# Performance work log

Measured on AMD Instinct MI355X. Metric: run time of the kernel, lower is better.

The kernel has to match this reference:

```python
import jax, jax.numpy as jnp
import numpy as np

D = 1024          # label_size / in_features
V = 100000        # vocab size
SHORTLIST = 10000 # cutoffs[0]
# tail clusters: (proj_dim, cluster_size) per div_value=2 schedule
TAILS = [(512, 10000), (256, 20000), (128, 40000), (64, 20000)]


def setup_inputs() -> dict:
    key = jax.random.key(0)
    ks = jax.random.split(key, 11)
    s = jnp.float32(0.02)
    inp = {
        "feature": jax.random.normal(ks[0], (D,), jnp.float32),
        "targets": jax.random.randint(ks[1], (4096,), 0, V),
        "head_w": jax.random.normal(ks[2], (SHORTLIST + len(TAILS), D), jnp.float32) * s,
    }
    for i, (h, c) in enumerate(TAILS):
        inp[f"t{i}p"] = jax.random.normal(ks[3 + 2 * i], (h, D), jnp.float32) * s
        inp[f"t{i}w"] = jax.random.normal(ks[4 + 2 * i], (c, h), jnp.float32) * s
    return inp


def reference(feature, targets, head_w, t0p, t0w, t1p, t1w, t2p, t2w, t3p, t3w):
    # head logits: [SHORTLIST + n_clusters]
    head_lp = jax.nn.log_softmax(head_w @ feature)
    parts = [head_lp[:SHORTLIST]]
    tails = [(t0p, t0w), (t1p, t1w), (t2p, t2w), (t3p, t3w)]
    for i, (p, w) in enumerate(tails):
        # two-stage low-rank projection: [h] then cluster logits [c]
        cl_lp = jax.nn.log_softmax(w @ (p @ feature)) + head_lp[SHORTLIST + i]
        parts.append(cl_lp)
    logprob = jnp.concatenate(parts)  # [V] full-vocab log-probabilities
    return -jnp.mean(logprob[targets])
```

## Files before the change

kernel.cpp:

```cpp
#include <hip/hip_runtime.h>
#include <math.h>

#define NHEAD     10004
#define OFF_HEAD  0
#define OFF_H0    10004
#define OFF_H1    10516
#define OFF_H2    10772
#define OFF_H3    10900
#define OFF_C0    10964
#define OFF_C1    20964
#define OFF_C2    40964
#define OFF_C3    80964
#define OFF_PH    100964
#define OFF_P0    101590
#define OFF_P1    102215
#define OFF_P2    103465
#define OFF_P3    105965

__device__ __forceinline__ float wave_sum(float v) {
  v += __shfl_xor(v, 32, 64);
  v += __shfl_xor(v, 16, 64);
  v += __shfl_xor(v, 8, 64);
  v += __shfl_xor(v, 4, 64);
  v += __shfl_xor(v, 2, 64);
  v += __shfl_xor(v, 1, 64);
  return v;
}

__global__ __launch_bounds__(256) void head_proj_kernel(
    const float* __restrict__ feat, const float* __restrict__ head_w,
    const float* __restrict__ p0, const float* __restrict__ p1,
    const float* __restrict__ p2, const float* __restrict__ p3,
    float* __restrict__ ws) {
  __shared__ __align__(16) float sf[1024];
  ((float4*)sf)[threadIdx.x] = ((const float4*)feat)[threadIdx.x];
  __syncthreads();
  const float4* sf4 = (const float4*)sf;
  const int wave = threadIdx.x >> 6, lane = threadIdx.x & 63;
  const int b = blockIdx.x;

  if (b < 626) {
    float esum = 0.f;
#pragma unroll
    for (int k = 0; k < 4; ++k) {
      int row = b * 16 + wave * 4 + k;
      if (row < NHEAD) {
        const float4* src4 = (const float4*)head_w + (size_t)row * 256;
        float acc = 0.f;
#pragma unroll
        for (int j = 0; j < 4; ++j) {
          float4 a = src4[lane + j * 64];
          float4 c = sf4[lane + j * 64];
          acc += a.x * c.x + a.y * c.y + a.z * c.z + a.w * c.w;
        }
        acc = wave_sum(acc);
        if (lane == 0) { ws[OFF_HEAD + row] = acc; esum += expf(acc); }
      }
    }
    __shared__ float wred[4];
    if (lane == 0) wred[wave] = esum;
    __syncthreads();
    if (threadIdx.x == 0) ws[OFF_PH + b] = wred[0] + wred[1] + wred[2] + wred[3];
  } else {
    const int pb = b - 626;
#pragma unroll
    for (int k = 0; k < 4; ++k) {
      int row = NHEAD + pb * 16 + wave * 4 + k;
      const float* src;
      if (row < 10516)      src = p0 + (size_t)(row - 10004) * 1024;
      else if (row < 10772) src = p1 + (size_t)(row - 10516) * 1024;
      else if (row < 10900) src = p2 + (size_t)(row - 10772) * 1024;
      else                  src = p3 + (size_t)(row - 10900) * 1024;
      const float4* src4 = (const float4*)src;
      float acc = 0.f;
#pragma unroll
      for (int j = 0; j < 4; ++j) {
        float4 a = src4[lane + j * 64];
        float4 c = sf4[lane + j * 64];
        acc += a.x * c.x + a.y * c.y + a.z * c.z + a.w * c.w;
      }
      acc = wave_sum(acc);
      if (lane == 0) ws[row] = acc;
    }
  }
}

__global__ __launch_bounds__(256) void tail_kernel(
    const float* __restrict__ w0, const float* __restrict__ w1,
    const float* __restrict__ w2, const float* __restrict__ w3,
    float* __restrict__ ws) {
  __shared__ __align__(16) float sh[512];
  const int b = blockIdx.x;
  const float* w; int h, hoff, coff, poff, lb;
  if (b < 625)       { w = w0; h = 512; hoff = OFF_H0; coff = OFF_C0; poff = OFF_P0; lb = b; }
  else if (b < 1875) { w = w1; h = 256; hoff = OFF_H1; coff = OFF_C1; poff = OFF_P1; lb = b - 625; }
  else if (b < 4375) { w = w2; h = 128; hoff = OFF_H2; coff = OFF_C2; poff = OFF_P2; lb = b - 1875; }
  else               { w = w3; h = 64;  hoff = OFF_H3; coff = OFF_C3; poff = OFF_P3; lb = b - 4375; }
  for (int t = threadIdx.x; t < h; t += 256) sh[t] = ws[hoff + t];
  __syncthreads();
  const int wave = threadIdx.x >> 6, lane = threadIdx.x & 63;
  const int row0 = lb * 16 + wave * 4;
  float esum = 0.f;
#pragma unroll
  for (int k = 0; k < 4; ++k) {
    int row = row0 + k;
    const float* wr = w + (size_t)row * h;
    float acc = 0.f;
    if (h == 512) {
      const float4* wr4 = (const float4*)wr; const float4* sh4 = (const float4*)sh;
#pragma unroll
      for (int j = 0; j < 2; ++j) {
        float4 a = wr4[lane + j * 64]; float4 c = sh4[lane + j * 64];
        acc += a.x * c.x + a.y * c.y + a.z * c.z + a.w * c.w;
      }
    } else if (h == 256) {
      float4 a = ((const float4*)wr)[lane]; float4 c = ((const float4*)sh)[lane];
      acc = a.x * c.x + a.y * c.y + a.z * c.z + a.w * c.w;
    } else if (h == 128) {
      float2 a = ((const float2*)wr)[lane]; float2 c = ((const float2*)sh)[lane];
      acc = a.x * c.x + a.y * c.y;
    } else {
      acc = wr[lane] * sh[lane];
    }
    acc = wave_sum(acc);
    if (lane == 0) { ws[coff + row] = acc; esum += expf(acc); }
  }
  __shared__ float wred[4];
  if (lane == 0) wred[wave] = esum;
  __syncthreads();
  if (threadIdx.x == 0) ws[poff + lb] = wred[0] + wred[1] + wred[2] + wred[3];
}

__global__ __launch_bounds__(256) void finalize_kernel(
    const int* __restrict__ targets, const float* __restrict__ ws,
    float* __restrict__ out) {
  __shared__ float red[256];
  float lse[5];
  const int offs[5] = {OFF_PH, OFF_P0, OFF_P1, OFF_P2, OFF_P3};
  const int lens[5] = {626, 625, 1250, 2500, 1250};
  for (int s = 0; s < 5; ++s) {
    float v = 0.f;
    for (int i = threadIdx.x; i < lens[s]; i += 256) v += ws[offs[s] + i];
    red[threadIdx.x] = v; __syncthreads();
    for (int st = 128; st; st >>= 1) {
      if (threadIdx.x < st) red[threadIdx.x] += red[threadIdx.x + st];
      __syncthreads();
    }
    lse[s] = logf(red[0]);
    __syncthreads();
  }
  const float clh0 = ws[10000] - lse[0];
  const float clh1 = ws[10001] - lse[0];
  const float clh2 = ws[10002] - lse[0];
  const float clh3 = ws[10003] - lse[0];
  float s = 0.f;
  for (int i = threadIdx.x; i < 4096; i += 256) {
    int t = targets[i]; float lp;
    if (t < 10000)      lp = ws[OFF_HEAD + t] - lse[0];
    else if (t < 20000) lp = ws[OFF_C0 + t - 10000] - lse[1] + clh0;
    else if (t < 40000) lp = ws[OFF_C1 + t - 20000] - lse[2] + clh1;
    else if (t < 80000) lp = ws[OFF_C2 + t - 40000] - lse[3] + clh2;
    else                lp = ws[OFF_C3 + t - 80000] - lse[4] + clh3;
    s += lp;
  }
  red[threadIdx.x] = s; __syncthreads();
  for (int st = 128; st; st >>= 1) {
    if (threadIdx.x < st) red[threadIdx.x] += red[threadIdx.x + st];
    __syncthreads();
  }
  if (threadIdx.x == 0) out[0] = -red[0] / 4096.f;
}

extern "C" void kernel_launch(void* const* d_in, const int* in_sizes, int n_in,
                              void* d_out, int out_size, void* d_ws, size_t ws_size,
                              hipStream_t stream) {
  const float* feat    = (const float*)d_in[0];
  const int*   targets = (const int*)d_in[1];
  const float* head_w  = (const float*)d_in[2];
  const float* t0p = (const float*)d_in[3];
  const float* t0w = (const float*)d_in[4];
  const float* t1p = (const float*)d_in[5];
  const float* t1w = (const float*)d_in[6];
  const float* t2p = (const float*)d_in[7];
  const float* t2w = (const float*)d_in[8];
  const float* t3p = (const float*)d_in[9];
  const float* t3w = (const float*)d_in[10];
  float* ws  = (float*)d_ws;
  float* out = (float*)d_out;

  head_proj_kernel<<<686, 256, 0, stream>>>(feat, head_w, t0p, t1p, t2p, t3p, ws);
  tail_kernel<<<5625, 256, 0, stream>>>(t0w, t1w, t2w, t3w, ws);
  finalize_kernel<<<1, 256, 0, stream>>>(targets, ws, out);
}
```

Baseline: 191.3 us.

## Replace per-block partials with atomics, batch row loads, parallelize final gather

Each block now adds its exp-sum partial straight into a global accumulator with atomicAdd, so the single-block finalize no longer has to reduce thousands of partials. The head and tail dot-product loops issue all row loads before computing, which raises memory-level parallelism. The target gather is spread over 16 blocks with an atomic sum, followed by a tiny writeout kernel and a zero-init kernel. This adds two extra launches and makes the float accumulation order nondeterministic.

```diff
diff --git a/kernel.cpp b/kernel.cpp
--- a/kernel.cpp
+++ b/kernel.cpp
@@ -11,11 +11,7 @@
 #define OFF_C1    20964
 #define OFF_C2    40964
 #define OFF_C3    80964
-#define OFF_PH    100964
-#define OFF_P0    101590
-#define OFF_P1    102215
-#define OFF_P2    103465
-#define OFF_P3    105965
+#define OFF_ACC   100964
 
 __device__ __forceinline__ float wave_sum(float v) {
   v += __shfl_xor(v, 32, 64);
@@ -25,6 +21,10 @@
   v += __shfl_xor(v, 2, 64);
   v += __shfl_xor(v, 1, 64);
   return v;
+}
+
+__global__ __launch_bounds__(64) void init_kernel(float* __restrict__ ws) {
+  if (threadIdx.x < 8) ws[OFF_ACC + threadIdx.x] = 0.f;
 }
 
 __global__ __launch_bounds__(256) void head_proj_kernel(
@@ -40,47 +40,54 @@
   const int b = blockIdx.x;
 
   if (b < 626) {
+    const int row0 = b * 16 + wave * 4;
+    float4 a[4][4];
+#pragma unroll
+    for (int k = 0; k < 4; ++k) {
+      int row = min(row0 + k, NHEAD - 1);
+      const float4* src4 = (const float4*)head_w + (size_t)row * 256;
+#pragma unroll
+      for (int j = 0; j < 4; ++j) a[k][j] = src4[lane + j * 64];
+    }
     float esum = 0.f;
 #pragma unroll
     for (int k = 0; k < 4; ++k) {
-      int row = b * 16 + wave * 4 + k;
-      if (row < NHEAD) {
-        const float4* src4 = (const float4*)head_w + (size_t)row * 256;
-        float acc = 0.f;
-#pragma unroll
-        for (int j = 0; j < 4; ++j) {
-          float4 a = src4[lane + j * 64];
-          float4 c = sf4[lane + j * 64];
-          acc += a.x * c.x + a.y * c.y + a.z * c.z + a.w * c.w;
-        }
-        acc = wave_sum(acc);
-        if (lane == 0) { ws[OFF_HEAD + row] = acc; esum += expf(acc); }
+      float acc = 0.f;
+#pragma unroll
+      for (int j = 0; j < 4; ++j) {
+        float4 c = sf4[lane + j * 64];
+        acc += a[k][j].x * c.x + a[k][j].y * c.y + a[k][j].z * c.z + a[k][j].w * c.w;
       }
-    }
-    __shared__ float wred[4];
-    if (lane == 0) wred[wave] = esum;
-    __syncthreads();
-    if (threadIdx.x == 0) ws[OFF_PH + b] = wred[0] + wred[1] + wred[2] + wred[3];
+      acc = wave_sum(acc);
+      if (lane == 0 && row0 + k < NHEAD) { ws[OFF_HEAD + row0 + k] = acc; esum += expf(acc); }
+    }
+    if (lane == 0) atomicAdd(&ws[OFF_ACC + 0], esum);
   } else {
     const int pb = b - 626;
-#pragma unroll
-    for (int k = 0; k < 4; ++k) {
-      int row = NHEAD + pb * 16 + wave * 4 + k;
+    const int row0 = NHEAD + pb * 16 + wave * 4;
+    float4 a[4][4];
+#pragma unroll
+    for (int k = 0; k < 4; ++k) {
+      int row = row0 + k;
       const float* src;
       if (row < 10516)      src = p0 + (size_t)(row - 10004) * 1024;
       else if (row < 10772) src = p1 + (size_t)(row - 10516) * 1024;
       else if (row < 10900) src = p2 + (size_t)(row - 10772) * 1024;
       else                  src = p3 + (size_t)(row - 10900) * 1024;
       const float4* src4 = (const float4*)src;
+#pragma unroll
+      for (int j = 0; j < 4; ++j) a[k][j] = src4[lane + j * 64];
+    }
+#pragma unroll
+    for (int k = 0; k < 4; ++k) {
       float acc = 0.f;
 #pragma unroll
       for (int j = 0; j < 4; ++j) {
-        float4 a = src4[lane + j * 64];
         float4 c = sf4[lane + j * 64];
-        acc += a.x * c.x + a.y * c.y + a.z * c.z + a.w * c.w;
+        acc += a[k][j].x * c.x + a[k][j].y * c.y + a[k][j].z * c.z + a[k][j].w * c.w;
       }
       acc = wave_sum(acc);
-      if (lane == 0) ws[row] = acc;
+      if (lane == 0) ws[row0 + k] = acc;
     }
   }
 }
@@ -91,84 +98,98 @@
     float* __restrict__ ws) {
   __shared__ __align__(16) float sh[512];
   const int b = blockIdx.x;
-  const float* w; int h, hoff, coff, poff, lb;
-  if (b < 625)       { w = w0; h = 512; hoff = OFF_H0; coff = OFF_C0; poff = OFF_P0; lb = b; }
-  else if (b < 1875) { w = w1; h = 256; hoff = OFF_H1; coff = OFF_C1; poff = OFF_P1; lb = b - 625; }
-  else if (b < 4375) { w = w2; h = 128; hoff = OFF_H2; coff = OFF_C2; poff = OFF_P2; lb = b - 1875; }
-  else               { w = w3; h = 64;  hoff = OFF_H3; coff = OFF_C3; poff = OFF_P3; lb = b - 4375; }
+  const float* w; int h, hoff, coff, ci, lb;
+  if (b < 625)       { w = w0; h = 512; hoff = OFF_H0; coff = OFF_C0; ci = 1; lb = b; }
+  else if (b < 1875) { w = w1; h = 256; hoff = OFF_H1; coff = OFF_C1; ci = 2; lb = b - 625; }
+  else if (b < 4375) { w = w2; h = 128; hoff = OFF_H2; coff = OFF_C2; ci = 3; lb = b - 1875; }
+  else               { w = w3; h = 64;  hoff = OFF_H3; coff = OFF_C3; ci = 4; lb = b - 4375; }
   for (int t = threadIdx.x; t < h; t += 256) sh[t] = ws[hoff + t];
   __syncthreads();
   const int wave = threadIdx.x >> 6, lane = threadIdx.x & 63;
   const int row0 = lb * 16 + wave * 4;
   float esum = 0.f;
-#pragma unroll
-  for (int k = 0; k < 4; ++k) {
-    int row = row0 + k;
-    const float* wr = w + (size_t)row * h;
-    float acc = 0.f;
-    if (h == 512) {
-      const float4* wr4 = (const float4*)wr; const float4* sh4 = (const float4*)sh;
+  if (h == 512) {
+    float4 a[4][2];
+#pragma unroll
+    for (int k = 0; k < 4; ++k) {
+      const float4* wr4 = (const float4*)(w + (size_t)(row0 + k) * 512);
+#pragma unroll
+      for (int j = 0; j < 2; ++j) a[k][j] = wr4[lane + j * 64];
+    }
+    const float4* sh4 = (const float4*)sh;
+#pragma unroll
+    for (int k = 0; k < 4; ++k) {
+      float acc = 0.f;
 #pragma unroll
       for (int j = 0; j < 2; ++j) {
-        float4 a = wr4[lane + j * 64]; float4 c = sh4[lane + j * 64];
-        acc += a.x * c.x + a.y * c.y + a.z * c.z + a.w * c.w;
+        float4 c = sh4[lane + j * 64];
+        acc += a[k][j].x * c.x + a[k][j].y * c.y + a[k][j].z * c.z + a[k][j].w * c.w;
       }
-    } else if (h == 256) {
-      float4 a = ((const float4*)wr)[lane]; float4 c = ((const float4*)sh)[lane];
-      acc = a.x * c.x + a.y * c.y + a.z * c.z + a.w * c.w;
-    } else if (h == 128) {
-      float2 a = ((const float2*)wr)[lane]; float2 c = ((const float2*)sh)[lane];
-      acc = a.x * c.x + a.y * c.y;
-    } else {
-      acc = wr[lane] * sh[lane];
-    }
-    acc = wave_sum(acc);
-    if (lane == 0) { ws[coff + row] = acc; esum += expf(acc); }
+      acc = wave_sum(acc);
+      if (lane == 0) { ws[coff + row0 + k] = acc; esum += expf(acc); }
+    }
+  } else if (h == 256) {
+    float4 a[4];
+#pragma unroll
+    for (int k = 0; k < 4; ++k) a[k] = ((const float4*)(w + (size_t)(row0 + k) * 256))[lane];
+    const float4 c = ((const float4*)sh)[lane];
+#pragma unroll
+    for (int k = 0; k < 4; ++k) {
+      float acc = a[k].x * c.x + a[k].y * c.y + a[k].z * c.z + a[k].w * c.w;
+      acc = wave_sum(acc);
+      if (lane == 0) { ws[coff + row0 + k] = acc; esum += expf(acc); }
+    }
+  } else if (h == 128) {
+    float2 a[4];
+#pragma unroll
+    for (int k = 0; k < 4; ++k) a[k] = ((const float2*)(w + (size_t)(row0 + k) * 128))[lane];
+    const float2 c = ((const float2*)sh)[lane];
+#pragma unroll
+    for (int k = 0; k < 4; ++k) {
+      float acc = a[k].x * c.x + a[k].y * c.y;
+      acc = wave_sum(acc);
+      if (lane == 0) { ws[coff + row0 + k] = acc; esum += expf(acc); }
+    }
+  } else {
+    float a[4];
+#pragma unroll
+    for (int k = 0; k < 4; ++k) a[k] = w[(size_t)(row0 + k) * 64 + lane];
+    const float c = sh[lane];
+#pragma unroll
+    for (int k = 0; k < 4; ++k) {
+      float acc = wave_sum(a[k] * c);
+      if (lane == 0) { ws[coff + row0 + k] = acc; esum += expf(acc); }
+    }
   }
+  if (lane == 0) atomicAdd(&ws[OFF_ACC + ci], esum);
+}
+
+__global__ __launch_bounds__(256) void gather_kernel(
+    const int* __restrict__ targets, float* __restrict__ ws) {
+  const float lse0 = logf(ws[OFF_ACC + 0]);
+  const float lse1 = logf(ws[OFF_ACC + 1]);
+  const float lse2 = logf(ws[OFF_ACC + 2]);
+  const float lse3 = logf(ws[OFF_ACC + 3]);
+  const float lse4 = logf(ws[OFF_ACC + 4]);
+  const int i = blockIdx.x * 256 + threadIdx.x;
+  const int t = targets[i];
+  float lp;
+  if (t < 10000)      lp = ws[OFF_HEAD + t] - lse0;
+  else if (t < 20000) lp = ws[OFF_C0 + t - 10000] - lse1 + (ws[10000] - lse0);
+  else if (t < 40000) lp = ws[OFF_C1 + t - 20000] - lse2 + (ws[10001] - lse0);
+  else if (t < 80000) lp = ws[OFF_C2 + t - 40000] - lse3 + (ws[10002] - lse0);
+  else                lp = ws[OFF_C3 + t - 80000] - lse4 + (ws[10003] - lse0);
+  float s = wave_sum(lp);
   __shared__ float wred[4];
-  if (lane == 0) wred[wave] = esum;
+  const int wave = threadIdx.x >> 6, lane = threadIdx.x & 63;
+  if (lane == 0) wred[wave] = s;
   __syncthreads();
-  if (threadIdx.x == 0) ws[poff + lb] = wred[0] + wred[1] + wred[2] + wred[3];
-}
-
-__global__ __launch_bounds__(256) void finalize_kernel(
-    const int* __restrict__ targets, const float* __restrict__ ws,
-    float* __restrict__ out) {
-  __shared__ float red[256];
-  float lse[5];
-  const int offs[5] = {OFF_PH, OFF_P0, OFF_P1, OFF_P2, OFF_P3};
-  const int lens[5] = {626, 625, 1250, 2500, 1250};
-  for (int s = 0; s < 5; ++s) {
-    float v = 0.f;
-    for (int i = threadIdx.x; i < lens[s]; i += 256) v += ws[offs[s] + i];
-    red[threadIdx.x] = v; __syncthreads();
-    for (int st = 128; st; st >>= 1) {
-      if (threadIdx.x < st) red[threadIdx.x] += red[threadIdx.x + st];
-      __syncthreads();
-    }
-    lse[s] = logf(red[0]);
-    __syncthreads();
-  }
-  const float clh0 = ws[10000] - lse[0];
-  const float clh1 = ws[10001] - lse[0];
-  const float clh2 = ws[10002] - lse[0];
-  const float clh3 = ws[10003] - lse[0];
-  float s = 0.f;
-  for (int i = threadIdx.x; i < 4096; i += 256) {
-    int t = targets[i]; float lp;
-    if (t < 10000)      lp = ws[OFF_HEAD + t] - lse[0];
-    else if (t < 20000) lp = ws[OFF_C0 + t - 10000] - lse[1] + clh0;
-    else if (t < 40000) lp = ws[OFF_C1 + t - 20000] - lse[2] + clh1;
-    else if (t < 80000) lp = ws[OFF_C2 + t - 40000] - lse[3] + clh2;
-    else                lp = ws[OFF_C3 + t - 80000] - lse[4] + clh3;
-    s += lp;
-  }
-  red[threadIdx.x] = s; __syncthreads();
-  for (int st = 128; st; st >>= 1) {
-    if (threadIdx.x < st) red[threadIdx.x] += red[threadIdx.x + st];
-    __syncthreads();
-  }
-  if (threadIdx.x == 0) out[0] = -red[0] / 4096.f;
+  if (threadIdx.x == 0) atomicAdd(&ws[OFF_ACC + 5], wred[0] + wred[1] + wred[2] + wred[3]);
+}
+
+__global__ __launch_bounds__(64) void writeout_kernel(
+    const float* __restrict__ ws, float* __restrict__ out) {
+  if (threadIdx.x == 0) out[0] = -ws[OFF_ACC + 5] * (1.f / 4096.f);
 }
 
 extern "C" void kernel_launch(void* const* d_in, const int* in_sizes, int n_in,
@@ -188,7 +209,9 @@
   float* ws  = (float*)d_ws;
   float* out = (float*)d_out;
 
+  init_kernel<<<1, 64, 0, stream>>>(ws);
   head_proj_kernel<<<686, 256, 0, stream>>>(feat, head_w, t0p, t1p, t2p, t3p, ws);
   tail_kernel<<<5625, 256, 0, stream>>>(t0w, t1w, t2w, t3w, ws);
-  finalize_kernel<<<1, 256, 0, stream>>>(targets, ws, out);
-}
+  gather_kernel<<<16, 256, 0, stream>>>(targets, ws);
+  writeout_kernel<<<1, 64, 0, stream>>>(ws, out);
+}
```

After: 458.0 us. +139.4%, slower.

## Specialize tail kernel per cluster with more rows per block, parallelize target gather

Applied to the files above, without the earlier changes.

Splits the tail kernel into one code path per cluster width. The narrower clusters now process 32 or 64 rows per block, which cuts the grid from 5625 to 2813 blocks and the number of partial sums. The single-block finalize is replaced by a 16-block gather kernel, where each block recomputes the five log-sum-exps and reduces its own slice of targets, plus a tiny writeout kernel that sums the 16 partials. This trades an extra launch and redundant LSE reductions for less serial work in the final step and fewer tiny blocks.

```diff
diff --git a/kernel.cpp b/kernel.cpp
--- a/kernel.cpp
+++ b/kernel.cpp
@@ -14,8 +14,9 @@
 #define OFF_PH    100964
 #define OFF_P0    101590
 #define OFF_P1    102215
-#define OFF_P2    103465
-#define OFF_P3    105965
+#define OFF_P2    102840
+#define OFF_P3    104090
+#define OFF_G     104403
 
 __device__ __forceinline__ float wave_sum(float v) {
   v += __shfl_xor(v, 32, 64);
@@ -90,54 +91,82 @@
     const float* __restrict__ w2, const float* __restrict__ w3,
     float* __restrict__ ws) {
   __shared__ __align__(16) float sh[512];
+  __shared__ float wred[4];
   const int b = blockIdx.x;
-  const float* w; int h, hoff, coff, poff, lb;
-  if (b < 625)       { w = w0; h = 512; hoff = OFF_H0; coff = OFF_C0; poff = OFF_P0; lb = b; }
-  else if (b < 1875) { w = w1; h = 256; hoff = OFF_H1; coff = OFF_C1; poff = OFF_P1; lb = b - 625; }
-  else if (b < 4375) { w = w2; h = 128; hoff = OFF_H2; coff = OFF_C2; poff = OFF_P2; lb = b - 1875; }
-  else               { w = w3; h = 64;  hoff = OFF_H3; coff = OFF_C3; poff = OFF_P3; lb = b - 4375; }
-  for (int t = threadIdx.x; t < h; t += 256) sh[t] = ws[hoff + t];
-  __syncthreads();
   const int wave = threadIdx.x >> 6, lane = threadIdx.x & 63;
-  const int row0 = lb * 16 + wave * 4;
   float esum = 0.f;
-#pragma unroll
-  for (int k = 0; k < 4; ++k) {
-    int row = row0 + k;
-    const float* wr = w + (size_t)row * h;
-    float acc = 0.f;
-    if (h == 512) {
-      const float4* wr4 = (const float4*)wr; const float4* sh4 = (const float4*)sh;
+  int poff, lb;
+
+  if (b < 625) {
+    lb = b; poff = OFF_P0;
+    for (int t = threadIdx.x; t < 512; t += 256) sh[t] = ws[OFF_H0 + t];
+    __syncthreads();
+    const float4* sh4 = (const float4*)sh;
+    const int row0 = lb * 16 + wave * 4;
+#pragma unroll
+    for (int k = 0; k < 4; ++k) {
+      const float4* wr4 = (const float4*)(w0 + (size_t)(row0 + k) * 512);
+      float acc = 0.f;
 #pragma unroll
       for (int j = 0; j < 2; ++j) {
         float4 a = wr4[lane + j * 64]; float4 c = sh4[lane + j * 64];
         acc += a.x * c.x + a.y * c.y + a.z * c.z + a.w * c.w;
       }
-    } else if (h == 256) {
-      float4 a = ((const float4*)wr)[lane]; float4 c = ((const float4*)sh)[lane];
-      acc = a.x * c.x + a.y * c.y + a.z * c.z + a.w * c.w;
-    } else if (h == 128) {
-      float2 a = ((const float2*)wr)[lane]; float2 c = ((const float2*)sh)[lane];
-      acc = a.x * c.x + a.y * c.y;
-    } else {
-      acc = wr[lane] * sh[lane];
-    }
-    acc = wave_sum(acc);
-    if (lane == 0) { ws[coff + row] = acc; esum += expf(acc); }
+      acc = wave_sum(acc);
+      if (lane == 0) { ws[OFF_C0 + row0 + k] = acc; esum += expf(acc); }
+    }
+  } else if (b < 1250) {
+    lb = b - 625; poff = OFF_P1;
+    if (threadIdx.x < 256) sh[threadIdx.x] = ws[OFF_H1 + threadIdx.x];
+    __syncthreads();
+    const float4 c = ((const float4*)sh)[lane];
+    const int row0 = lb * 32 + wave * 8;
+#pragma unroll
+    for (int k = 0; k < 8; ++k) {
+      float4 a = ((const float4*)(w1 + (size_t)(row0 + k) * 256))[lane];
+      float acc = a.x * c.x + a.y * c.y + a.z * c.z + a.w * c.w;
+      acc = wave_sum(acc);
+      if (lane == 0) { ws[OFF_C1 + row0 + k] = acc; esum += expf(acc); }
+    }
+  } else if (b < 2500) {
+    lb = b - 1250; poff = OFF_P2;
+    if (threadIdx.x < 128) sh[threadIdx.x] = ws[OFF_H2 + threadIdx.x];
+    __syncthreads();
+    const float2 c = ((const float2*)sh)[lane];
+    const int row0 = lb * 32 + wave * 8;
+#pragma unroll
+    for (int k = 0; k < 8; ++k) {
+      float2 a = ((const float2*)(w2 + (size_t)(row0 + k) * 128))[lane];
+      float acc = a.x * c.x + a.y * c.y;
+      acc = wave_sum(acc);
+      if (lane == 0) { ws[OFF_C2 + row0 + k] = acc; esum += expf(acc); }
+    }
+  } else {
+    lb = b - 2500; poff = OFF_P3;
+    if (threadIdx.x < 64) sh[threadIdx.x] = ws[OFF_H3 + threadIdx.x];
+    __syncthreads();
+    const float c = sh[lane];
+    const int row0 = lb * 64 + wave * 16;
+#pragma unroll
+    for (int k = 0; k < 16; ++k) {
+      int row = row0 + k;
+      int rc = min(row, 19999);
+      float a = w3[(size_t)rc * 64 + lane];
+      float acc = wave_sum(a * c);
+      if (lane == 0 && row < 20000) { ws[OFF_C3 + row] = acc; esum += expf(acc); }
+    }
   }
-  __shared__ float wred[4];
   if (lane == 0) wred[wave] = esum;
   __syncthreads();
   if (threadIdx.x == 0) ws[poff + lb] = wred[0] + wred[1] + wred[2] + wred[3];
 }
 
-__global__ __launch_bounds__(256) void finalize_kernel(
-    const int* __restrict__ targets, const float* __restrict__ ws,
-    float* __restrict__ out) {
+__global__ __launch_bounds__(256) void gather_kernel(
+    const int* __restrict__ targets, float* __restrict__ ws) {
   __shared__ float red[256];
-  float lse[5];
+  __shared__ float slse[5];
   const int offs[5] = {OFF_PH, OFF_P0, OFF_P1, OFF_P2, OFF_P3};
-  const int lens[5] = {626, 625, 1250, 2500, 1250};
+  const int lens[5] = {626, 625, 625, 1250, 313};
   for (int s = 0; s < 5; ++s) {
     float v = 0.f;
     for (int i = threadIdx.x; i < lens[s]; i += 256) v += ws[offs[s] + i];
@@ -146,29 +175,31 @@
       if (threadIdx.x < st) red[threadIdx.x] += red[threadIdx.x + st];
       __syncthreads();
     }
-    lse[s] = logf(red[0]);
+    if (threadIdx.x == 0) slse[s] = logf(red[0]);
     __syncthreads();
   }
-  const float clh0 = ws[10000] - lse[0];
-  const float clh1 = ws[10001] - lse[0];
-  const float clh2 = ws[10002] - lse[0];
-  const float clh3 = ws[10003] - lse[0];
-  float s = 0.f;
-  for (int i = threadIdx.x; i < 4096; i += 256) {
-    int t = targets[i]; float lp;
-    if (t < 10000)      lp = ws[OFF_HEAD + t] - lse[0];
-    else if (t < 20000) lp = ws[OFF_C0 + t - 10000] - lse[1] + clh0;
-    else if (t < 40000) lp = ws[OFF_C1 + t - 20000] - lse[2] + clh1;
-    else if (t < 80000) lp = ws[OFF_C2 + t - 40000] - lse[3] + clh2;
-    else                lp = ws[OFF_C3 + t - 80000] - lse[4] + clh3;
-    s += lp;
-  }
-  red[threadIdx.x] = s; __syncthreads();
-  for (int st = 128; st; st >>= 1) {
-    if (threadIdx.x < st) red[threadIdx.x] += red[threadIdx.x + st];
-    __syncthreads();
-  }
-  if (threadIdx.x == 0) out[0] = -red[0] / 4096.f;
+  const float lse0 = slse[0], lse1 = slse[1], lse2 = slse[2], lse3 = slse[3], lse4 = slse[4];
+  const int i = blockIdx.x * 256 + threadIdx.x;
+  const int t = targets[i];
+  float lp;
+  if (t < 10000)      lp = ws[OFF_HEAD + t] - lse0;
+  else if (t < 20000) lp = ws[OFF_C0 + t - 10000] - lse1 + (ws[10000] - lse0);
+  else if (t < 40000) lp = ws[OFF_C1 + t - 20000] - lse2 + (ws[10001] - lse0);
+  else if (t < 80000) lp = ws[OFF_C2 + t - 40000] - lse3 + (ws[10002] - lse0);
+  else                lp = ws[OFF_C3 + t - 80000] - lse4 + (ws[10003] - lse0);
+  float s = wave_sum(lp);
+  __shared__ float wred[4];
+  const int wave = threadIdx.x >> 6, lane = threadIdx.x & 63;
+  if (lane == 0) wred[wave] = s;
+  __syncthreads();
+  if (threadIdx.x == 0) ws[OFF_G + blockIdx.x] = wred[0] + wred[1] + wred[2] + wred[3];
+}
+
+__global__ __launch_bounds__(64) void writeout_kernel(
+    const float* __restrict__ ws, float* __restrict__ out) {
+  float v = (threadIdx.x < 16) ? ws[OFF_G + threadIdx.x] : 0.f;
+  v = wave_sum(v);
+  if (threadIdx.x == 0) out[0] = -v * (1.f / 4096.f);
 }
 
 extern "C" void kernel_launch(void* const* d_in, const int* in_sizes, int n_in,
@@ -189,6 +220,7 @@
   float* out = (float*)d_out;
 
   head_proj_kernel<<<686, 256, 0, stream>>>(feat, head_w, t0p, t1p, t2p, t3p, ws);
-  tail_kernel<<<5625, 256, 0, stream>>>(t0w, t1w, t2w, t3w, ws);
-  finalize_kernel<<<1, 256, 0, stream>>>(targets, ws, out);
-}
+  tail_kernel<<<2813, 256, 0, stream>>>(t0w, t1w, t2w, t3w, ws);
+  gather_kernel<<<16, 256, 0, stream>>>(targets, ws);
+  writeout_kernel<<<1, 64, 0, stream>>>(ws, out);
+}
```

New measurement: 170.4 us. 1.12x faster.
